# Optimization experiments

Measured on AMD Instinct MI355X. Metric: run time of the kernel, lower is better.

## Reference

```python
import jax, jax.numpy as jnp
import numpy as np

B, S, D, H, I = 4, 1024, 2048, 16, 8192
HD = D // H
S_IMG = 576
EPS = 1e-5


def _layer_norm(x, w, b):
    mu = jnp.mean(x, axis=-1, keepdims=True)
    var = jnp.var(x, axis=-1, keepdims=True)
    return (x - mu) * jax.lax.rsqrt(var + EPS) * w + b


def setup_inputs() -> dict:
    key = jax.random.key(0)
    ks = jax.random.split(key, 12)
    s = 0.02
    return {
        "image_features": jax.random.normal(ks[0], (B, S_IMG, D), jnp.float32),
        "hidden_states": jax.random.normal(ks[1], (B, S, D), jnp.float32),
        "attention_mask": jnp.ones((B, S), jnp.float32),
        "causal_attention_mask": jnp.zeros((B, 1, S, S), jnp.float32),
        "Wq": jax.random.normal(ks[2], (D, D), jnp.float32) * s,
        "bq": jnp.zeros((D,), jnp.float32),
        "Wk": jax.random.normal(ks[3], (D, D), jnp.float32) * s,
        "bk": jnp.zeros((D,), jnp.float32),
        "Wv": jax.random.normal(ks[4], (D, D), jnp.float32) * s,
        "bv": jnp.zeros((D,), jnp.float32),
        "Wo": jax.random.normal(ks[5], (D, D), jnp.float32) * s,
        "bo": jnp.zeros((D,), jnp.float32),
        "ln1_w": jnp.ones((D,), jnp.float32),
        "ln1_b": jnp.zeros((D,), jnp.float32),
        "ln2_w": jnp.ones((D,), jnp.float32),
        "ln2_b": jnp.zeros((D,), jnp.float32),
        "W1": jax.random.normal(ks[6], (I, D), jnp.float32) * s,
        "b1": jnp.zeros((I,), jnp.float32),
        "W2": jax.random.normal(ks[7], (D, I), jnp.float32) * s,
        "b2": jnp.zeros((D,), jnp.float32),
    }


def reference(image_features, hidden_states, attention_mask, causal_attention_mask,
              Wq, bq, Wk, bk, Wv, bv, Wo, bo,
              ln1_w, ln1_b, ln2_w, ln2_b, W1, b1, W2, b2):
    dtype = hidden_states.dtype
    scale = HD ** (-0.5)
    # expand_mask: [B,S] -> additive mask [B,1,S,S]
    inverted = 1.0 - attention_mask[:, None, None, :].astype(dtype)  # [B,1,1,S]
    add_mask = jnp.where(inverted.astype(bool), jnp.finfo(dtype).min, inverted)
    add_mask = jnp.broadcast_to(add_mask, (B, 1, S, S))

    residual = hidden_states
    x = _layer_norm(hidden_states, ln1_w, ln1_b)

    q = (x @ Wq.T + bq) * scale
    k = x @ Wk.T + bk
    v = x @ Wv.T + bv
    q = q.reshape(B, S, H, HD)
    k = k.reshape(B, S, H, HD)
    v = v.reshape(B, S, H, HD)

    scores = jnp.einsum('bqhd,bkhd->bhqk', q, k) + add_mask  # [B,H,S,S]
    probs = jax.nn.softmax(scores, axis=-1)
    attn = jnp.einsum('bhqk,bkhd->bqhd', probs, v).reshape(B, S, D)
    attn = attn @ Wo.T + bo

    hidden = residual + attn
    residual = hidden
    y = _layer_norm(hidden, ln2_w, ln2_b)
    y = jax.nn.gelu(y @ W1.T + b1, approximate=False)
    y = y @ W2.T + b2
    return residual + y
```

## Files before the change

kernel.cpp:

```cpp
#include <hip/hip_runtime.h>
#include <hip/hip_bf16.h>
#include <math.h>

typedef __hip_bfloat16 bf16;
typedef __attribute__((ext_vector_type(8))) short short8;
typedef __attribute__((ext_vector_type(4))) float floatx4;

constexpr int Bc = 4, Sc = 1024, Dc = 2048, Hc = 16, HDc = 128, Ic = 8192;
constexpr int QKVLD = 3 * Dc;

__device__ __forceinline__ float bf2f(bf16 x){ return __bfloat162float(x); }
__device__ __forceinline__ bf16 f2bf(float x){ return __float2bfloat16(x); }

__device__ __forceinline__ uint4 pack8(float4 a, float4 b){
    union { uint4 u; bf16 h[8]; } r;
    r.h[0]=f2bf(a.x); r.h[1]=f2bf(a.y); r.h[2]=f2bf(a.z); r.h[3]=f2bf(a.w);
    r.h[4]=f2bf(b.x); r.h[5]=f2bf(b.y); r.h[6]=f2bf(b.z); r.h[7]=f2bf(b.w);
    return r.u;
}

__device__ __forceinline__ void glds16(void* lds, const void* g){
    __builtin_amdgcn_global_load_lds(
        (__attribute__((address_space(1))) void*)(size_t)g,
        (__attribute__((address_space(3))) void*)lds,
        16, 0, 0);
}

__global__ __launch_bounds__(256)
void conv_w(const float* __restrict__ src, bf16* __restrict__ dst){
    const size_t i = ((size_t)blockIdx.x * 256 + threadIdx.x) * 8;
    float4 a = *(const float4*)(src + i);
    float4 b = *(const float4*)(src + i + 4);
    *(uint4*)(dst + i) = pack8(a, b);
}

__global__ __launch_bounds__(256)
void conv_w4(const float* __restrict__ s0, const float* __restrict__ s1,
             const float* __restrict__ s2, const float* __restrict__ s3,
             bf16* __restrict__ dst){
    const int id = blockIdx.x >> 11;
    const float* src = (id == 0) ? s0 : (id == 1) ? s1 : (id == 2) ? s2 : s3;
    const size_t i = ((size_t)(blockIdx.x & 2047) * 256 + threadIdx.x) * 8;
    float4 a = *(const float4*)(src + i);
    float4 b = *(const float4*)(src + i + 4);
    *(uint4*)(dst + (size_t)id * Dc * Dc + i) = pack8(a, b);
}

__global__ __launch_bounds__(256)
void init_add(float* __restrict__ dst, const float* __restrict__ bias,
              const float* __restrict__ src){
    const size_t i = ((size_t)blockIdx.x * 256 + threadIdx.x) * 8;
    const int col = (int)(i & (Dc - 1));
    float4 a = *(const float4*)(src + i);
    float4 b = *(const float4*)(src + i + 4);
    float4 ba = *(const float4*)(bias + col);
    float4 bb = *(const float4*)(bias + col + 4);
    a.x += ba.x; a.y += ba.y; a.z += ba.z; a.w += ba.w;
    b.x += bb.x; b.y += bb.y; b.z += bb.z; b.w += bb.w;
    *(float4*)(dst + i) = a;
    *(float4*)(dst + i + 4) = b;
}

template<int INF32>
__global__ __launch_bounds__(256)
void ln_kernel(const void* __restrict__ x, const float* __restrict__ w,
               const float* __restrict__ b, bf16* __restrict__ y)
{
    const int row = blockIdx.x;
    const int t = threadIdx.x;
    float f[8], s = 0.f, s2 = 0.f;
    if (INF32) {
        const float* xr = (const float*)x + (size_t)row * Dc + t * 8;
        float4 a = *(const float4*)xr, c = *(const float4*)(xr + 4);
        f[0]=a.x; f[1]=a.y; f[2]=a.z; f[3]=a.w; f[4]=c.x; f[5]=c.y; f[6]=c.z; f[7]=c.w;
    } else {
        union { uint4 u; bf16 h[8]; } ld;
        ld.u = *(const uint4*)((const bf16*)x + (size_t)row * Dc + t * 8);
#pragma unroll
        for (int j = 0; j < 8; ++j) f[j] = bf2f(ld.h[j]);
    }
#pragma unroll
    for (int j = 0; j < 8; ++j) { s += f[j]; s2 += f[j] * f[j]; }
#pragma unroll
    for (int off = 32; off; off >>= 1) { s += __shfl_xor(s, off); s2 += __shfl_xor(s2, off); }
    __shared__ float red[8];
    const int wave = t >> 6, lane = t & 63;
    if (lane == 0) { red[wave] = s; red[4 + wave] = s2; }
    __syncthreads();
    s  = red[0] + red[1] + red[2] + red[3];
    s2 = red[4] + red[5] + red[6] + red[7];
    const float mean = s * (1.0f / Dc);
    const float var  = s2 * (1.0f / Dc) - mean * mean;
    const float rs   = rsqrtf(var + 1e-5f);
    union { uint4 u; bf16 h[8]; } st;
#pragma unroll
    for (int j = 0; j < 8; ++j) {
        const int col = t * 8 + j;
        st.h[j] = f2bf((f[j] - mean) * rs * w[col] + b[col]);
    }
    *(uint4*)&y[(size_t)row * Dc + t * 8] = st.u;
}


#define BAR()   __builtin_amdgcn_s_barrier()
#define LGKM0() asm volatile("s_waitcnt lgkmcnt(0)" ::: "memory")
#define VMW2()  asm volatile("s_waitcnt vmcnt(2)" ::: "memory")
#define VMW0()  asm volatile("s_waitcnt vmcnt(0)" ::: "memory")
#define SCB0()  __builtin_amdgcn_sched_barrier(0)
#define PRIO(x) __builtin_amdgcn_s_setprio(x)

template<int EPI, int RESF32, int OUTF32>
__global__ __launch_bounds__(512, 2)
void gemm_bt(const bf16* __restrict__ A, const bf16* __restrict__ W,
             const float* __restrict__ bias, const float* __restrict__ bias2,
             const float* __restrict__ bias3, const void* __restrict__ res,
             void* __restrict__ C, int M, int N, int K, float scale)
{
    __shared__ __align__(16) char lds[131072];

    const int nwgx = gridDim.x;
    const int nwg  = nwgx * gridDim.y;
    int bid = blockIdx.y * nwgx + blockIdx.x;
    bid = (bid & 7) * (nwg >> 3) + (bid >> 3);
    const int tile_n = (bid % nwgx) * 256;
    const int tile_m = (bid / nwgx) * 256;

    const int t = threadIdx.x;
    const int wave = t >> 6, lane = t & 63, quad = lane >> 4, l16 = lane & 15;
    const int wmp = wave >> 2, wnp = wave & 3;
    const int Klen = K / gridDim.z, kbeg = blockIdx.z * Klen;
    const int NT = Klen >> 6;

    const int g8  = lane & 7;
    const int lr0 = wave * 16 + (lane >> 3);
    const int lr1 = lr0 + 8;
    const int c0 = (g8 - lr0) & 7, c1 = (g8 - lr1) & 7;
    const size_t aof0 = (size_t)(tile_m + (lr0 >> 6) * 128 + (lr0 & 63)) * K + kbeg + c0 * 8;
    const size_t aof1 = (size_t)(tile_m + (lr1 >> 6) * 128 + (lr1 & 63)) * K + kbeg + c1 * 8;
    const size_t bof0 = (size_t)(tile_n + lr0) * K + kbeg + c0 * 8;
    const size_t bof1 = (size_t)(tile_n + lr1) * K + kbeg + c1 * 8;
    const int ls0 = wave * 2048, ls1 = wave * 2048 + 1024;

    const int ard = (wmp * 64 + l16) * 128;
    const int brd = 32768 + (wnp * 64 + l16) * 128;
    const int gq0 = ((quad + l16) & 7) * 16;

    floatx4 acc[8][4] = {};
    short8 av[4], bv0[4], bv1[4];

#define STAGE_A(_b, _mh, _kt) do { \
    glds16(lds + (_b) * 65536 + (_mh) * 16384 + ls0, \
           A + aof0 + (size_t)((_mh) * 64) * K + (_kt) * 64); \
    glds16(lds + (_b) * 65536 + (_mh) * 16384 + ls1, \
           A + aof1 + (size_t)((_mh) * 64) * K + (_kt) * 64); \
} while (0)

#define STAGE_B(_b, _h, _kt) do { \
    glds16(lds + (_b) * 65536 + 32768 + (_h) * 16384 + ls0, \
           W + bof0 + (size_t)((_h) * 128) * K + (_kt) * 64); \
    glds16(lds + (_b) * 65536 + 32768 + (_h) * 16384 + ls1, \
           W + bof1 + (size_t)((_h) * 128) * K + (_kt) * 64); \
} while (0)

#define LDA4(_b, _mh, _ks) do { \
    const char* _p = lds + (_b) * 65536 + (_mh) * 16384 + ard + (gq0 ^ ((_ks) * 64)); \
    av[0] = *(const short8*)(_p);        av[1] = *(const short8*)(_p + 2048); \
    av[2] = *(const short8*)(_p + 4096); av[3] = *(const short8*)(_p + 6144); \
} while (0)

#define LDB4(_b, _ks, _arr) do { \
    const char* _p = lds + (_b) * 65536 + brd + (gq0 ^ ((_ks) * 64)); \
    _arr[0] = *(const short8*)(_p);        _arr[1] = *(const short8*)(_p + 2048); \
    _arr[2] = *(const short8*)(_p + 4096); _arr[3] = *(const short8*)(_p + 6144); \
} while (0)

#define MFB(_mh, _bv) do { \
    _Pragma("unroll") \
    for (int _mi = 0; _mi < 4; ++_mi) { \
        _Pragma("unroll") \
        for (int _ni = 0; _ni < 4; ++_ni) \
            acc[(_mh) * 4 + _mi][_ni] = __builtin_amdgcn_mfma_f32_16x16x32_bf16( \
                av[_mi], _bv[_ni], acc[(_mh) * 4 + _mi][_ni], 0, 0, 0); \
    } \
} while (0)

#define TILE(_bb, _tt) do { \
     \
    if ((_tt) + 1 < NT) { STAGE_A((_bb) ^ 1, 1, (_tt) + 1); STAGE_B((_bb) ^ 1, 0, (_tt) + 1); } \
    LDA4(_bb, 0, 0); LDB4(_bb, 0, bv0); \
    BAR(); LGKM0(); SCB0(); PRIO(1); MFB(0, bv0); PRIO(0); BAR(); \
     \
    if ((_tt) + 1 < NT) STAGE_B((_bb) ^ 1, 1, (_tt) + 1); \
    LDA4(_bb, 0, 1); LDB4(_bb, 1, bv1); \
    BAR(); LGKM0(); SCB0(); PRIO(1); MFB(0, bv1); PRIO(0); BAR(); \
     \
    if ((_tt) + 2 < NT) STAGE_A(_bb, 0, (_tt) + 2); \
    LDA4(_bb, 1, 0); \
    BAR(); LGKM0(); SCB0(); PRIO(1); MFB(1, bv0); PRIO(0); BAR(); \
     \
    LDA4(_bb, 1, 1); \
    BAR(); LGKM0(); SCB0(); PRIO(1); MFB(1, bv1); PRIO(0); \
    if ((_tt) + 2 < NT)      { VMW2(); } \
    else if ((_tt) + 1 < NT) { VMW0(); } \
    BAR(); \
} while (0)

    STAGE_A(0, 0, 0); STAGE_A(0, 1, 0);
    STAGE_B(0, 0, 0); STAGE_B(0, 1, 0);
    STAGE_A(1, 0, 1);
    VMW2();
    BAR();

    for (int tt = 0; tt < NT; tt += 2) {
        TILE(0, tt);
        TILE(1, tt + 1);
    }

#undef TILE
#undef MFB
#undef LDB4
#undef LDA4
#undef STAGE_B
#undef STAGE_A

#pragma unroll
    for (int mi = 0; mi < 8; ++mi) {
        const int row0 = tile_m + wmp * 128 + mi * 16 + quad * 4;
#pragma unroll
        for (int ni = 0; ni < 4; ++ni) {
            const int col = tile_n + wnp * 64 + ni * 16 + l16;
            float bv = 0.f, sc = 1.f;
            if (EPI == 4) {
                if (col < 2048)      { bv = bias[col];         sc = scale; }
                else if (col < 4096) { bv = bias2[col - 2048]; }
                else                 { bv = bias3[col - 4096]; }
            } else if (EPI != 5) {
                bv = bias[col];
            }
#pragma unroll
            for (int r = 0; r < 4; ++r) {
                const size_t idx = (size_t)(row0 + r) * N + col;
                float v = acc[mi][ni][r];
                if (EPI == 5) { atomicAdd(&((float*)C)[idx], v); continue; }
                v += bv;
                if (EPI == 1) v *= scale;
                if (EPI == 4) v *= sc;
                if (EPI == 2) v = 0.5f * v * (1.0f + erff(v * 0.70710678118f));
                if (EPI == 3) v += RESF32 ? ((const float*)res)[idx] : bf2f(((const bf16*)res)[idx]);
                if (OUTF32) ((float*)C)[idx] = v;
                else        ((bf16*)C)[idx] = f2bf(v);
            }
        }
    }
}

__global__ __launch_bounds__(256)
void flash_attn(const bf16* __restrict__ QKV, const float* __restrict__ mask,
                bf16* __restrict__ O)
{
    __shared__ __align__(16) bf16 Ks[4 * 64 * 32];
    __shared__ __align__(16) bf16 Vt[128 * 72];
    __shared__ __align__(16) bf16 Ps[4][16 * 72];
    const int bh = blockIdx.y, b = bh >> 4, h = bh & 15;
    const int t = threadIdx.x, w = t >> 6, lane = t & 63, quad = lane >> 4, l16 = lane & 15;
    const int qbase = blockIdx.x * 64 + w * 16;
    const size_t rowb = (size_t)b * Sc;
    const bf16* Kp = QKV + 2048 + (size_t)h * HDc;
    const bf16* Vp = QKV + 4096 + (size_t)h * HDc;

    short8 qf[4];
    {
        const bf16* qp = QKV + (rowb + qbase + l16) * QKVLD + (size_t)h * HDc + quad * 8;
#pragma unroll
        for (int kc = 0; kc < 4; ++kc) qf[kc] = *(const short8*)(qp + kc * 32);
    }
    float m_i[4], l_i[4];
    floatx4 Oacc[8] = {};
#pragma unroll
    for (int r = 0; r < 4; ++r) { m_i[r] = -1e30f; l_i[r] = 0.f; }

    const int p2 = t & 31, dg = t >> 5;

    for (int kt = 0; kt < Sc; kt += 64) {
        __syncthreads();
#pragma unroll
        for (int u = 0; u < 4; ++u) {
            const int row = u * 16 + (lane >> 2);
            glds16((char*)Ks + w * 4096 + u * 1024,
                   Kp + (rowb + kt + row) * QKVLD + w * 32 + (lane & 3) * 8);
        }
        {
            union { uint4 u4; unsigned short s[8]; } va[2][2];
#pragma unroll
            for (int kk = 0; kk < 2; ++kk) {
                const bf16* vp = Vp + (rowb + kt + 2 * p2 + kk) * QKVLD + dg * 16;
                va[kk][0].u4 = *(const uint4*)vp;
                va[kk][1].u4 = *(const uint4*)(vp + 8);
            }
            unsigned* VtW = (unsigned*)Vt;
#pragma unroll
            for (int j = 0; j < 16; ++j) {
                const unsigned word = (unsigned)va[0][j >> 3].s[j & 7]
                                    | ((unsigned)va[1][j >> 3].s[j & 7] << 16);
                VtW[(dg * 16 + j) * 36 + p2] = word;
            }
        }
        __syncthreads();

        floatx4 sacc[4] = {};
#pragma unroll
        for (int kc = 0; kc < 4; ++kc)
#pragma unroll
            for (int sub = 0; sub < 4; ++sub) {
                short8 kf = *(const short8*)&Ks[kc * 2048 + (sub * 16 + l16) * 32 + quad * 8];
                sacc[sub] = __builtin_amdgcn_mfma_f32_16x16x32_bf16(qf[kc], kf, sacc[sub], 0, 0, 0);
            }
#pragma unroll
        for (int sub = 0; sub < 4; ++sub) {
            const float mv = mask[b * Sc + kt + sub * 16 + l16];
            const float madd = (mv < 0.5f) ? -3.0e38f : 0.f;
#pragma unroll
            for (int r = 0; r < 4; ++r) sacc[sub][r] += madd;
        }
        float p[4][4], alpha[4];
#pragma unroll
        for (int r = 0; r < 4; ++r) {
            float mx = fmaxf(fmaxf(sacc[0][r], sacc[1][r]), fmaxf(sacc[2][r], sacc[3][r]));
#pragma unroll
            for (int off = 8; off; off >>= 1) mx = fmaxf(mx, __shfl_xor(mx, off));
            const float mnew = fmaxf(m_i[r], mx);
            alpha[r] = exp2f(m_i[r] - mnew);
            float ps = 0.f;
#pragma unroll
            for (int sub = 0; sub < 4; ++sub) { p[sub][r] = exp2f(sacc[sub][r] - mnew); ps += p[sub][r]; }
#pragma unroll
            for (int off = 8; off; off >>= 1) ps += __shfl_xor(ps, off);
            l_i[r] = l_i[r] * alpha[r] + ps;
            m_i[r] = mnew;
        }
#pragma unroll
        for (int nsub = 0; nsub < 8; ++nsub)
#pragma unroll
            for (int r = 0; r < 4; ++r) Oacc[nsub][r] *= alpha[r];

        bf16* Pw = Ps[w];
#pragma unroll
        for (int sub = 0; sub < 4; ++sub)
#pragma unroll
            for (int r = 0; r < 4; ++r)
                Pw[(quad * 4 + r) * 72 + sub * 16 + l16] = f2bf(p[sub][r]);
        const short8 pf0 = *(const short8*)&Pw[l16 * 72 + quad * 8];
        const short8 pf1 = *(const short8*)&Pw[l16 * 72 + 32 + quad * 8];
#pragma unroll
        for (int nsub = 0; nsub < 8; ++nsub) {
            const short8 vf0 = *(const short8*)&Vt[(nsub * 16 + l16) * 72 + quad * 8];
            const short8 vf1 = *(const short8*)&Vt[(nsub * 16 + l16) * 72 + 32 + quad * 8];
            Oacc[nsub] = __builtin_amdgcn_mfma_f32_16x16x32_bf16(pf0, vf0, Oacc[nsub], 0, 0, 0);
            Oacc[nsub] = __builtin_amdgcn_mfma_f32_16x16x32_bf16(pf1, vf1, Oacc[nsub], 0, 0, 0);
        }
    }

#pragma unroll
    for (int r = 0; r < 4; ++r) {
        const float inv = 1.f / l_i[r];
        bf16* orow = O + (rowb + qbase + quad * 4 + r) * Dc + (size_t)h * HDc;
#pragma unroll
        for (int nsub = 0; nsub < 8; ++nsub)
            orow[nsub * 16 + l16] = f2bf(Oacc[nsub][r] * inv);
    }
}

extern "C" void kernel_launch(void* const* d_in, const int* in_sizes, int n_in,
                              void* d_out, int out_size, void* d_ws, size_t ws_size,
                              hipStream_t stream)
{
    const float* hidden = (const float*)d_in[1];
    const float* amask  = (const float*)d_in[2];
    const float* Wq = (const float*)d_in[4];  const float* bq = (const float*)d_in[5];
    const float* Wk = (const float*)d_in[6];  const float* bk = (const float*)d_in[7];
    const float* Wv = (const float*)d_in[8];  const float* bv = (const float*)d_in[9];
    const float* Wo = (const float*)d_in[10]; const float* bo = (const float*)d_in[11];
    const float* ln1w = (const float*)d_in[12]; const float* ln1b = (const float*)d_in[13];
    const float* ln2w = (const float*)d_in[14]; const float* ln2b = (const float*)d_in[15];
    const float* W1 = (const float*)d_in[16]; const float* b1 = (const float*)d_in[17];
    const float* W2 = (const float*)d_in[18]; const float* b2 = (const float*)d_in[19];

    const size_t UE = 8ull * 1024 * 1024;
    const size_t WE = 4ull * 1024 * 1024;
    bf16*  U = (bf16*)d_ws;
    bf16*  qkv   = U;
    bf16*  wbuf  = U + 4 * UE;
    bf16*  x_ln  = U + 6 * UE;
    float* hid2f = (float*)(U + 6 * UE);
    bf16*  ffn1  = U;
    bf16*  attn  = (bf16*)d_out;
    bf16*  y_ln  = (bf16*)d_out + UE;
    float* outf  = (float*)d_out;

    const float qscale = 0.08838834764831845f * 1.4426950408889634f;
    const dim3 gQKV(QKVLD / 256, Bc * Sc / 256, 1);
    const dim3 gWo (Dc / 256,    Bc * Sc / 256, 2);
    const dim3 gF1 (Ic / 256,    Bc * Sc / 256, 1);
    const dim3 gF2 (Dc / 256,    Bc * Sc / 256, 2);

    conv_w4<<<8192, 256, 0, stream>>>(Wq, Wk, Wv, Wo, wbuf);
    ln_kernel<1><<<Bc * Sc, 256, 0, stream>>>(hidden, ln1w, ln1b, x_ln);
    gemm_bt<4,0,0><<<gQKV, 512, 0, stream>>>(x_ln, wbuf, bq, bk, bv, nullptr, qkv,
                                             Bc * Sc, QKVLD, Dc, qscale);
    flash_attn<<<dim3(Sc / 64, Bc * Hc), 256, 0, stream>>>(qkv, amask, attn);
    init_add<<<4096, 256, 0, stream>>>(hid2f, bo, hidden);
    gemm_bt<5,0,1><<<gWo, 512, 0, stream>>>(attn, wbuf + 3 * WE, nullptr, nullptr, nullptr,
                                            nullptr, hid2f, Bc * Sc, Dc, Dc, 0.f);
    ln_kernel<1><<<Bc * Sc, 256, 0, stream>>>(hid2f, ln2w, ln2b, y_ln);
    conv_w<<<8192, 256, 0, stream>>>(W1, wbuf);
    gemm_bt<2,0,0><<<gF1, 512, 0, stream>>>(y_ln, wbuf, b1, nullptr, nullptr, nullptr, ffn1,
                                            Bc * Sc, Ic, Dc, 0.f);
    init_add<<<4096, 256, 0, stream>>>(outf, b2, hid2f);
    conv_w<<<8192, 256, 0, stream>>>(W2, wbuf);
    gemm_bt<5,0,1><<<gF2, 512, 0, stream>>>(ffn1, wbuf, nullptr, nullptr, nullptr,
                                            nullptr, outf, Bc * Sc, Dc, Ic, 0.f);
}
```

Baseline: 948.3 us.

## Add 128x256 GEMM variant, replace split-K atomics with fused residual epilogue

Adds a half-height GEMM kernel (128-row M tiles, 96 KB LDS) and uses it for the QKV, Wo and FFN2 projections. Wo and FFN2 no longer run split-K with atomicAdd into a buffer pre-filled by init_add. Each output tile now does the full K loop and writes bias plus residual directly. This removes two init_add launches, the extra residual read/write traffic and the atomic contention. In exchange the smaller tiles reuse each loaded operand less, and FFN2 loses split-K parallelism over K=8192.

```diff
diff --git a/kernel.cpp b/kernel.cpp
--- a/kernel.cpp
+++ b/kernel.cpp
@@ -44,21 +44,6 @@
     float4 a = *(const float4*)(src + i);
     float4 b = *(const float4*)(src + i + 4);
     *(uint4*)(dst + (size_t)id * Dc * Dc + i) = pack8(a, b);
-}
-
-__global__ __launch_bounds__(256)
-void init_add(float* __restrict__ dst, const float* __restrict__ bias,
-              const float* __restrict__ src){
-    const size_t i = ((size_t)blockIdx.x * 256 + threadIdx.x) * 8;
-    const int col = (int)(i & (Dc - 1));
-    float4 a = *(const float4*)(src + i);
-    float4 b = *(const float4*)(src + i + 4);
-    float4 ba = *(const float4*)(bias + col);
-    float4 bb = *(const float4*)(bias + col + 4);
-    a.x += ba.x; a.y += ba.y; a.z += ba.z; a.w += ba.w;
-    b.x += bb.x; b.y += bb.y; b.z += bb.z; b.w += bb.w;
-    *(float4*)(dst + i) = a;
-    *(float4*)(dst + i + 4) = b;
 }
 
 template<int INF32>
@@ -101,10 +86,10 @@
     *(uint4*)&y[(size_t)row * Dc + t * 8] = st.u;
 }
 
-
 #define BAR()   __builtin_amdgcn_s_barrier()
 #define LGKM0() asm volatile("s_waitcnt lgkmcnt(0)" ::: "memory")
 #define VMW2()  asm volatile("s_waitcnt vmcnt(2)" ::: "memory")
+#define VMW1()  asm volatile("s_waitcnt vmcnt(1)" ::: "memory")
 #define VMW0()  asm volatile("s_waitcnt vmcnt(0)" ::: "memory")
 #define SCB0()  __builtin_amdgcn_sched_barrier(0)
 #define PRIO(x) __builtin_amdgcn_s_setprio(x)
@@ -185,19 +170,15 @@
 } while (0)
 
 #define TILE(_bb, _tt) do { \
-     \
     if ((_tt) + 1 < NT) { STAGE_A((_bb) ^ 1, 1, (_tt) + 1); STAGE_B((_bb) ^ 1, 0, (_tt) + 1); } \
     LDA4(_bb, 0, 0); LDB4(_bb, 0, bv0); \
     BAR(); LGKM0(); SCB0(); PRIO(1); MFB(0, bv0); PRIO(0); BAR(); \
-     \
     if ((_tt) + 1 < NT) STAGE_B((_bb) ^ 1, 1, (_tt) + 1); \
     LDA4(_bb, 0, 1); LDB4(_bb, 1, bv1); \
     BAR(); LGKM0(); SCB0(); PRIO(1); MFB(0, bv1); PRIO(0); BAR(); \
-     \
     if ((_tt) + 2 < NT) STAGE_A(_bb, 0, (_tt) + 2); \
     LDA4(_bb, 1, 0); \
     BAR(); LGKM0(); SCB0(); PRIO(1); MFB(1, bv0); PRIO(0); BAR(); \
-     \
     LDA4(_bb, 1, 1); \
     BAR(); LGKM0(); SCB0(); PRIO(1); MFB(1, bv1); PRIO(0); \
     if ((_tt) + 2 < NT)      { VMW2(); } \
@@ -226,6 +207,139 @@
 #pragma unroll
     for (int mi = 0; mi < 8; ++mi) {
         const int row0 = tile_m + wmp * 128 + mi * 16 + quad * 4;
+#pragma unroll
+        for (int ni = 0; ni < 4; ++ni) {
+            const int col = tile_n + wnp * 64 + ni * 16 + l16;
+            float bv = 0.f, sc = 1.f;
+            if (EPI == 4) {
+                if (col < 2048)      { bv = bias[col];         sc = scale; }
+                else if (col < 4096) { bv = bias2[col - 2048]; }
+                else                 { bv = bias3[col - 4096]; }
+            } else if (EPI != 5) {
+                bv = bias[col];
+            }
+#pragma unroll
+            for (int r = 0; r < 4; ++r) {
+                const size_t idx = (size_t)(row0 + r) * N + col;
+                float v = acc[mi][ni][r];
+                if (EPI == 5) { atomicAdd(&((float*)C)[idx], v); continue; }
+                v += bv;
+                if (EPI == 1) v *= scale;
+                if (EPI == 4) v *= sc;
+                if (EPI == 2) v = 0.5f * v * (1.0f + erff(v * 0.70710678118f));
+                if (EPI == 3) v += RESF32 ? ((const float*)res)[idx] : bf2f(((const bf16*)res)[idx]);
+                if (OUTF32) ((float*)C)[idx] = v;
+                else        ((bf16*)C)[idx] = f2bf(v);
+            }
+        }
+    }
+}
+
+template<int EPI, int RESF32, int OUTF32>
+__global__ __launch_bounds__(512, 2)
+void gemm_bt_h(const bf16* __restrict__ A, const bf16* __restrict__ W,
+               const float* __restrict__ bias, const float* __restrict__ bias2,
+               const float* __restrict__ bias3, const void* __restrict__ res,
+               void* __restrict__ C, int M, int N, int K, float scale)
+{
+    __shared__ __align__(16) char lds[98304];
+
+    const int nwgx = gridDim.x;
+    const int nwg  = nwgx * gridDim.y;
+    int bid = blockIdx.y * nwgx + blockIdx.x;
+    bid = (bid & 7) * (nwg >> 3) + (bid >> 3);
+    const int tile_n = (bid % nwgx) * 256;
+    const int tile_m = (bid / nwgx) * 128;
+
+    const int t = threadIdx.x;
+    const int wave = t >> 6, lane = t & 63, quad = lane >> 4, l16 = lane & 15;
+    const int wmp = wave >> 2, wnp = wave & 3;
+    const int NT = K >> 6;
+
+    const int arow = wave * 8 + (lane >> 3);
+    const int ca   = ((lane & 7) - arow) & 7;
+    const size_t aofh = (size_t)(tile_m + arow) * K + ca * 8;
+    const size_t bofh = (size_t)(tile_n + arow) * K + ca * 8;
+    const int lsw = wave * 1024;
+
+    const int ard = wmp * 8192 + l16 * 128;
+    const int brd = 16384 + (wnp * 64 + l16) * 128;
+    const int gq0 = ((quad + l16) & 7) * 16;
+
+    floatx4 acc[4][4] = {};
+    short8 av0[4], av1[4], bv0[4], bv1[4];
+
+#define STAGEH_A(_b, _mh, _kt) \
+    glds16(lds + (_b) * 49152 + (_mh) * 8192 + lsw, \
+           A + aofh + (size_t)((_mh) * 64) * K + (_kt) * 64)
+
+#define STAGEH_B(_b, _h, _kt) do { \
+    glds16(lds + (_b) * 49152 + 16384 + (_h) * 16384 + lsw, \
+           W + bofh + (size_t)((_h) * 128) * K + (_kt) * 64); \
+    glds16(lds + (_b) * 49152 + 16384 + (_h) * 16384 + 8192 + lsw, \
+           W + bofh + (size_t)((_h) * 128 + 64) * K + (_kt) * 64); \
+} while (0)
+
+#define LDAH(_b, _ks, _arr) do { \
+    const char* _p = lds + (_b) * 49152 + ard + (gq0 ^ ((_ks) * 64)); \
+    _arr[0] = *(const short8*)(_p);        _arr[1] = *(const short8*)(_p + 2048); \
+    _arr[2] = *(const short8*)(_p + 4096); _arr[3] = *(const short8*)(_p + 6144); \
+} while (0)
+
+#define LDBH(_b, _ks, _arr) do { \
+    const char* _p = lds + (_b) * 49152 + brd + (gq0 ^ ((_ks) * 64)); \
+    _arr[0] = *(const short8*)(_p);        _arr[1] = *(const short8*)(_p + 2048); \
+    _arr[2] = *(const short8*)(_p + 4096); _arr[3] = *(const short8*)(_p + 6144); \
+} while (0)
+
+#define MF8(_av, _bv, _n0, _n1) do { \
+    _Pragma("unroll") \
+    for (int _mi = 0; _mi < 4; ++_mi) { \
+        acc[_mi][_n0] = __builtin_amdgcn_mfma_f32_16x16x32_bf16(_av[_mi], _bv[_n0], acc[_mi][_n0], 0, 0, 0); \
+        acc[_mi][_n1] = __builtin_amdgcn_mfma_f32_16x16x32_bf16(_av[_mi], _bv[_n1], acc[_mi][_n1], 0, 0, 0); \
+    } \
+} while (0)
+
+#define TILEH(_bb, _tt) do { \
+     \
+    if ((_tt) + 1 < NT) STAGEH_A((_bb) ^ 1, 1, (_tt) + 1); \
+    LDAH(_bb, 0, av0); LDBH(_bb, 0, bv0); \
+    BAR(); LGKM0(); SCB0(); PRIO(1); MF8(av0, bv0, 0, 1); PRIO(0); BAR(); \
+     \
+    if ((_tt) + 1 < NT) { STAGEH_B((_bb) ^ 1, 0, (_tt) + 1); STAGEH_B((_bb) ^ 1, 1, (_tt) + 1); } \
+    LDAH(_bb, 1, av1); LDBH(_bb, 1, bv1); \
+    BAR(); LGKM0(); SCB0(); PRIO(1); MF8(av0, bv0, 2, 3); PRIO(0); BAR(); \
+     \
+    if ((_tt) + 2 < NT) STAGEH_A(_bb, 0, (_tt) + 2); \
+    BAR(); LGKM0(); SCB0(); PRIO(1); MF8(av1, bv1, 0, 1); PRIO(0); BAR(); \
+     \
+    BAR(); SCB0(); PRIO(1); MF8(av1, bv1, 2, 3); PRIO(0); \
+    if ((_tt) + 2 < NT)      { VMW1(); } \
+    else if ((_tt) + 1 < NT) { VMW0(); } \
+    BAR(); \
+} while (0)
+
+    STAGEH_A(0, 0, 0); STAGEH_A(0, 1, 0);
+    STAGEH_B(0, 0, 0); STAGEH_B(0, 1, 0);
+    STAGEH_A(1, 0, 1);
+    VMW1();
+    BAR();
+
+    for (int tt = 0; tt < NT; tt += 2) {
+        TILEH(0, tt);
+        TILEH(1, tt + 1);
+    }
+
+#undef TILEH
+#undef MF8
+#undef LDBH
+#undef LDAH
+#undef STAGEH_B
+#undef STAGEH_A
+
+#pragma unroll
+    for (int mi = 0; mi < 4; ++mi) {
+        const int row0 = tile_m + wmp * 64 + mi * 16 + quad * 4;
 #pragma unroll
         for (int ni = 0; ni < 4; ++ni) {
             const int col = tile_n + wnp * 64 + ni * 16 + l16;
@@ -398,25 +512,23 @@
     float* outf  = (float*)d_out;
 
     const float qscale = 0.08838834764831845f * 1.4426950408889634f;
-    const dim3 gQKV(QKVLD / 256, Bc * Sc / 256, 1);
-    const dim3 gWo (Dc / 256,    Bc * Sc / 256, 2);
+    const dim3 gQKV(QKVLD / 256, Bc * Sc / 128, 1);
+    const dim3 gWo (Dc / 256,    Bc * Sc / 128, 1);
     const dim3 gF1 (Ic / 256,    Bc * Sc / 256, 1);
-    const dim3 gF2 (Dc / 256,    Bc * Sc / 256, 2);
+    const dim3 gF2 (Dc / 256,    Bc * Sc / 128, 1);
 
     conv_w4<<<8192, 256, 0, stream>>>(Wq, Wk, Wv, Wo, wbuf);
     ln_kernel<1><<<Bc * Sc, 256, 0, stream>>>(hidden, ln1w, ln1b, x_ln);
-    gemm_bt<4,0,0><<<gQKV, 512, 0, stream>>>(x_ln, wbuf, bq, bk, bv, nullptr, qkv,
-                                             Bc * Sc, QKVLD, Dc, qscale);
+    gemm_bt_h<4,0,0><<<gQKV, 512, 0, stream>>>(x_ln, wbuf, bq, bk, bv, nullptr, qkv,
+                                               Bc * Sc, QKVLD, Dc, qscale);
     flash_attn<<<dim3(Sc / 64, Bc * Hc), 256, 0, stream>>>(qkv, amask, attn);
-    init_add<<<4096, 256, 0, stream>>>(hid2f, bo, hidden);
-    gemm_bt<5,0,1><<<gWo, 512, 0, stream>>>(attn, wbuf + 3 * WE, nullptr, nullptr, nullptr,
-                                            nullptr, hid2f, Bc * Sc, Dc, Dc, 0.f);
+    gemm_bt_h<3,1,1><<<gWo, 512, 0, stream>>>(attn, wbuf + 3 * WE, bo, nullptr, nullptr,
+                                              hidden, hid2f, Bc * Sc, Dc, Dc, 0.f);
     ln_kernel<1><<<Bc * Sc, 256, 0, stream>>>(hid2f, ln2w, ln2b, y_ln);
     conv_w<<<8192, 256, 0, stream>>>(W1, wbuf);
     gemm_bt<2,0,0><<<gF1, 512, 0, stream>>>(y_ln, wbuf, b1, nullptr, nullptr, nullptr, ffn1,
                                             Bc * Sc, Ic, Dc, 0.f);
-    init_add<<<4096, 256, 0, stream>>>(outf, b2, hid2f);
     conv_w<<<8192, 256, 0, stream>>>(W2, wbuf);
-    gemm_bt<5,0,1><<<gF2, 512, 0, stream>>>(ffn1, wbuf, nullptr, nullptr, nullptr,
-                                            nullptr, outf, Bc * Sc, Dc, Ic, 0.f);
-}
+    gemm_bt_h<3,1,1><<<gF2, 512, 0, stream>>>(ffn1, wbuf, b2, nullptr, nullptr,
+                                              hid2f, outf, Bc * Sc, Dc, Ic, 0.f);
+}
```

Measured after the change: 878.8 us. 7.3% less time.
